# Performance work log

Measured on AMD Instinct MI355X. Metric: run time of the kernel, lower is better.

Reference implementation:

```python
import jax, jax.numpy as jnp
import numpy as np

D_MODEL = 384
HEADS = 8
DIM_HEAD = D_MODEL // HEADS
IH = IW = 32
N = IH * IW
D_FF = 1536
EPS = 1e-5


def _relative_index():
    # replicates torch buffer construction (meshgrid 'ij')
    gy, gx = np.meshgrid(np.arange(IH), np.arange(IW), indexing='ij')
    coords = np.stack([gy, gx]).reshape(2, -1)              # [2, N]
    rel = coords[:, :, None] - coords[:, None, :]           # [2, N, N]
    rel[0] += IH - 1
    rel[1] += IW - 1
    rel[0] *= 2 * IW - 1
    return (rel[0] + rel[1]).reshape(-1)                    # [N*N] int


def setup_inputs() -> dict:
    key = jax.random.key(0)
    ks = jax.random.split(key, 16)
    s = 0.02
    return {
        'src': jax.random.normal(ks[0], (8, N, D_MODEL), jnp.float32),
        'pos': jax.random.normal(ks[1], (8, N, D_MODEL), jnp.float32),
        'rel_bias_table': jax.random.normal(ks[2], ((2 * IH - 1) * (2 * IW - 1), HEADS), jnp.float32) * s,
        'Wq': jax.random.normal(ks[3], (D_MODEL, D_MODEL), jnp.float32) * s,
        'Wk': jax.random.normal(ks[4], (D_MODEL, D_MODEL), jnp.float32) * s,
        'Wv': jax.random.normal(ks[5], (D_MODEL, D_MODEL), jnp.float32) * s,
        'Wo': jax.random.normal(ks[6], (D_MODEL, D_MODEL), jnp.float32) * s,
        'bo': jnp.zeros((D_MODEL,), jnp.float32),
        'W1': jax.random.normal(ks[7], (D_MODEL, D_FF), jnp.float32) * s,
        'b1': jnp.zeros((D_FF,), jnp.float32),
        'W2': jax.random.normal(ks[8], (D_FF, D_MODEL), jnp.float32) * s,
        'b2': jnp.zeros((D_MODEL,), jnp.float32),
        'g1': jnp.ones((D_MODEL,), jnp.float32),
        'be1': jnp.zeros((D_MODEL,), jnp.float32),
        'g2': jnp.ones((D_MODEL,), jnp.float32),
        'be2': jnp.zeros((D_MODEL,), jnp.float32),
    }


def _layernorm(x, g, b):
    mu = jnp.mean(x, -1, keepdims=True)
    var = jnp.var(x, -1, keepdims=True)
    return (x - mu) * jax.lax.rsqrt(var + EPS) * g + b


def _heads(x):
    b, n, _ = x.shape
    return x.reshape(b, n, HEADS, DIM_HEAD).transpose(0, 2, 1, 3)  # [b,h,n,d]


def reference(src, pos, rel_bias_table, Wq, Wk, Wv, Wo, bo, W1, b1, W2, b2, g1, be1, g2, be2):
    rel_idx = _relative_index()
    qk_in = src + pos
    q = _heads(qk_in @ Wq)
    k = _heads(qk_in @ Wk)
    v = _heads(src @ Wv)
    # relative bias: [heads, n, n]
    bias = rel_bias_table[rel_idx].reshape(N, N, HEADS).transpose(2, 0, 1)
    # relative_bias_x = (x^T @ bias)^T  ==  sum_m bias[h,m,n] * x[b,h,m,d]
    q = q + jnp.einsum('hmn,bhmd->bhnd', bias, q)
    k = k + jnp.einsum('hmn,bhmd->bhnd', bias, k)
    v = v + jnp.einsum('hmn,bhmd->bhnd', bias, v)
    scale = DIM_HEAD ** -0.5
    dots = jnp.einsum('bhnd,bhmd->bhnm', q, k) * scale
    attn = jax.nn.softmax(dots, axis=-1)
    out = jnp.einsum('bhnm,bhmd->bhnd', attn, v)
    out = out.transpose(0, 2, 1, 3).reshape(src.shape[0], N, D_MODEL)
    out = out @ Wo + bo
    x = _layernorm(src + out, g1, be1)
    ff = jax.nn.gelu(x @ W1 + b1, approximate=False) @ W2 + b2
    return _layernorm(x + ff, g2, be2)
```

## Files before the change

kernel.cpp:

```cpp
#include <hip/hip_runtime.h>
#include <math.h>

#define D_MODEL 384
#define HEADS 8
#define DIM_HEAD 48
#define NTOK 1024
#define BATCH 8
#define D_FF 1536
#define LN_EPS 1e-5f

typedef unsigned short u16;
typedef unsigned int u32;
typedef unsigned long long u64;
typedef short short8 __attribute__((ext_vector_type(8)));
typedef float f32x4 __attribute__((ext_vector_type(4)));

union F8 { short8 v; u64 q[2]; u16 u[8]; uint4 u4; };

__device__ __forceinline__ u16 f2bf(float f) {
    union { float f; unsigned u; } c; c.f = f;
    unsigned r = c.u + 0x7FFFu + ((c.u >> 16) & 1u);
    return (u16)(r >> 16);
}
__device__ __forceinline__ float bf2f(u16 u) {
    union { unsigned u; float f; } c; c.u = ((unsigned)u) << 16; return c.f;
}

__global__ __launch_bounds__(256) void add_cast_kernel(
        const float4* __restrict__ a, const float4* __restrict__ b,
        ushort4* __restrict__ o1, ushort4* __restrict__ o2, int n4) {
    int i = blockIdx.x * blockDim.x + threadIdx.x;
    if (i >= n4) return;
    float4 x = a[i], y = b[i];
    ushort4 u1, u2;
    u1.x = f2bf(x.x + y.x); u1.y = f2bf(x.y + y.y); u1.z = f2bf(x.z + y.z); u1.w = f2bf(x.w + y.w);
    u2.x = f2bf(x.x); u2.y = f2bf(x.y); u2.z = f2bf(x.z); u2.w = f2bf(x.w);
    o1[i] = u1; o2[i] = u2;
}

__global__ __launch_bounds__(256) void castT4_kernel(
        const float* __restrict__ i0, const float* __restrict__ i1,
        const float* __restrict__ i2, const float* __restrict__ i3,
        u16* __restrict__ o0, u16* __restrict__ o1,
        u16* __restrict__ o2, u16* __restrict__ o3) {
    const float* in  = (blockIdx.z == 0) ? i0 : (blockIdx.z == 1) ? i1 : (blockIdx.z == 2) ? i2 : i3;
    u16*         out = (blockIdx.z == 0) ? o0 : (blockIdx.z == 1) ? o1 : (blockIdx.z == 2) ? o2 : o3;
    __shared__ float t[32][33];
    int c0 = blockIdx.x * 32, r0 = blockIdx.y * 32;
    int tx = threadIdx.x, ty = threadIdx.y;
    for (int i = ty; i < 32; i += 8)
        t[i][tx] = in[(long)(r0 + i) * 384 + c0 + tx];
    __syncthreads();
    for (int i = ty; i < 32; i += 8)
        out[(long)(c0 + i) * 384 + r0 + tx] = f2bf(t[tx][i]);
}

__global__ __launch_bounds__(256) void castT_kernel(
        const float* __restrict__ in, u16* __restrict__ out, int R, int C) {
    __shared__ float t[32][33];
    int c0 = blockIdx.x * 32, r0 = blockIdx.y * 32;
    int tx = threadIdx.x, ty = threadIdx.y;
    for (int i = ty; i < 32; i += 8)
        t[i][tx] = in[(long)(r0 + i) * C + c0 + tx];
    __syncthreads();
    for (int i = ty; i < 32; i += 8)
        out[(long)(c0 + i) * R + r0 + tx] = f2bf(t[tx][i]);
}

__global__ __launch_bounds__(256) void biasT_bf16_kernel(const float* __restrict__ table,
                                                         u16* __restrict__ BT) {
    long i = (long)blockIdx.x * blockDim.x + threadIdx.x;
    const long total = (long)HEADS * NTOK * NTOK;
    if (i >= total) return;
    int m = (int)(i & 1023);
    int n = (int)((i >> 10) & 1023);
    int h = (int)(i >> 20);
    int dy = (m >> 5) - (n >> 5) + 31;
    int dx = (m & 31) - (n & 31) + 31;
    BT[i] = f2bf(table[(dy * 63 + dx) * HEADS + h]);
}

template<int OUTMODE, bool HAS_BIAS, bool HAS_RES, bool GELU_>
__global__ __launch_bounds__(256) void mgemm_kernel(
        const u16* __restrict__ Ab, const u16* __restrict__ Btb,
        float* __restrict__ Cf, u16* __restrict__ Cb, u16* __restrict__ Ct,
        const float* __restrict__ bias, const float* __restrict__ Rb,
        int M, int Kd, int Nd, int lda, int ldbt, int ldc, int ldr) {
    const u16* A  = Ab;
    const u16* Bt = Btb;

    __shared__ u16 As[64][40];
    __shared__ u16 Bs[64][40];
    int tid = threadIdx.x;
    int wave = tid >> 6, lane = tid & 63, g = lane >> 4, l15 = lane & 15;
    int wm = wave >> 1, wn = wave & 1;
    int row0 = blockIdx.y * 64, col0 = blockIdx.x * 64;

    f32x4 acc[2][2] = {};

    int sr = tid >> 2, sch = tid & 3;
    const u16* aSrc = A + (long)(row0 + sr) * lda + sch * 8;
    const u16* bSrc = Bt + (long)(col0 + sr) * ldbt + sch * 8;

    for (int k0 = 0; k0 < Kd; k0 += 32) {
        {
            uint4 va = *(const uint4*)(aSrc + k0);
            uint4 vb = *(const uint4*)(bSrc + k0);
            *(u64*)&As[sr][sch * 8]     = ((const u64*)&va)[0];
            *(u64*)&As[sr][sch * 8 + 4] = ((const u64*)&va)[1];
            *(u64*)&Bs[sr][sch * 8]     = ((const u64*)&vb)[0];
            *(u64*)&Bs[sr][sch * 8 + 4] = ((const u64*)&vb)[1];
        }
        __syncthreads();
        F8 af[2], bfr[2];
#pragma unroll
        for (int fm = 0; fm < 2; ++fm) {
            int r = wm * 32 + fm * 16 + l15;
            af[fm].q[0] = *(const u64*)&As[r][g * 8];
            af[fm].q[1] = *(const u64*)&As[r][g * 8 + 4];
        }
#pragma unroll
        for (int fn = 0; fn < 2; ++fn) {
            int c = wn * 32 + fn * 16 + l15;
            bfr[fn].q[0] = *(const u64*)&Bs[c][g * 8];
            bfr[fn].q[1] = *(const u64*)&Bs[c][g * 8 + 4];
        }
#pragma unroll
        for (int fm = 0; fm < 2; ++fm)
#pragma unroll
            for (int fn = 0; fn < 2; ++fn)
                acc[fm][fn] = __builtin_amdgcn_mfma_f32_16x16x32_bf16(
                    af[fm].v, bfr[fn].v, acc[fm][fn], 0, 0, 0);
        __syncthreads();
    }

#pragma unroll
    for (int fm = 0; fm < 2; ++fm) {
        int rbase = row0 + wm * 32 + fm * 16 + g * 4;
#pragma unroll
        for (int fn = 0; fn < 2; ++fn) {
            int c = col0 + wn * 32 + fn * 16 + l15;
            if (c < Nd) {
                float bv = HAS_BIAS ? bias[c] : 0.f;
                float vs[4];
#pragma unroll
                for (int r = 0; r < 4; ++r) {
                    float v = acc[fm][fn][r] + bv;
                    if (HAS_RES) v += Rb[(long)(rbase + r) * ldr + c];
                    if (GELU_)   v = 0.5f * v * (1.f + erff(v * 0.70710678118654752f));
                    vs[r] = v;
                    if (OUTMODE & 1) Cf[(long)(rbase + r) * ldc + c] = v;
                    if (OUTMODE & 2) Cb[(long)(rbase + r) * ldc + c] = f2bf(v);
                }
                if (OUTMODE & 8) {
                    int hh2 = (c * 683) >> 15; int dd = c - hh2 * 48;
                    int bb2 = rbase >> 10;     int mm = rbase & 1023;
                    ushort4 o;
                    o.x = f2bf(vs[0]); o.y = f2bf(vs[1]); o.z = f2bf(vs[2]); o.w = f2bf(vs[3]);
                    *(ushort4*)&Ct[(long)hh2 * 393216 + (long)(bb2 * 48 + dd) * 1024 + mm] = o;
                }
            }
        }
    }
}

__global__ __launch_bounds__(256) void bias3_kernel(
        const u16* __restrict__ BT, const u16* __restrict__ QtH,
        const u16* __restrict__ KtH, const u16* __restrict__ VtH,
        u16* __restrict__ Q2H, u16* __restrict__ K2H, u16* __restrict__ V2T) {
    int bid = blockIdx.x;
    int widx = (bid & 7) * 96 + (bid >> 3);
    int h = widx / 96;
    int rem = widx - h * 96;
    int ry = rem / 6, cx = rem - ry * 6;
    const long hb = (long)h * 393216;
    const u16* A = BT + (long)h * 1048576;
    __shared__ u16 As[64][40];
    __shared__ u16 Bq[64][40], Bk[64][40], Bv[64][40];
    int tid = threadIdx.x, wave = tid >> 6, lane = tid & 63, g = lane >> 4, l15 = lane & 15;
    int wm = wave >> 1, wn = wave & 1;
    int row0 = ry * 64, col0 = cx * 64;
    f32x4 acc[3][2][2] = {};
    int sr = tid >> 2, sch = tid & 3;
    const u16* aSrc = A   + (long)(row0 + sr) * 1024 + sch * 8;
    const u16* qSrc = QtH + hb + (long)(col0 + sr) * 1024 + sch * 8;
    const u16* kSrc = KtH + hb + (long)(col0 + sr) * 1024 + sch * 8;
    const u16* vSrc = VtH + hb + (long)(col0 + sr) * 1024 + sch * 8;

    for (int k0 = 0; k0 < 1024; k0 += 32) {
        uint4 va = *(const uint4*)(aSrc + k0);
        uint4 vq = *(const uint4*)(qSrc + k0);
        uint4 vk = *(const uint4*)(kSrc + k0);
        uint4 vv = *(const uint4*)(vSrc + k0);
        *(u64*)&As[sr][sch * 8] = ((const u64*)&va)[0]; *(u64*)&As[sr][sch * 8 + 4] = ((const u64*)&va)[1];
        *(u64*)&Bq[sr][sch * 8] = ((const u64*)&vq)[0]; *(u64*)&Bq[sr][sch * 8 + 4] = ((const u64*)&vq)[1];
        *(u64*)&Bk[sr][sch * 8] = ((const u64*)&vk)[0]; *(u64*)&Bk[sr][sch * 8 + 4] = ((const u64*)&vk)[1];
        *(u64*)&Bv[sr][sch * 8] = ((const u64*)&vv)[0]; *(u64*)&Bv[sr][sch * 8 + 4] = ((const u64*)&vv)[1];
        __syncthreads();
        F8 af0, af1, b0, b1;
        af0.q[0] = *(const u64*)&As[wm * 32 + l15][g * 8];
        af0.q[1] = *(const u64*)&As[wm * 32 + l15][g * 8 + 4];
        af1.q[0] = *(const u64*)&As[wm * 32 + 16 + l15][g * 8];
        af1.q[1] = *(const u64*)&As[wm * 32 + 16 + l15][g * 8 + 4];
        b0.q[0] = *(const u64*)&Bq[wn * 32 + l15][g * 8];
        b0.q[1] = *(const u64*)&Bq[wn * 32 + l15][g * 8 + 4];
        b1.q[0] = *(const u64*)&Bq[wn * 32 + 16 + l15][g * 8];
        b1.q[1] = *(const u64*)&Bq[wn * 32 + 16 + l15][g * 8 + 4];
        acc[0][0][0] = __builtin_amdgcn_mfma_f32_16x16x32_bf16(af0.v, b0.v, acc[0][0][0], 0, 0, 0);
        acc[0][0][1] = __builtin_amdgcn_mfma_f32_16x16x32_bf16(af0.v, b1.v, acc[0][0][1], 0, 0, 0);
        acc[0][1][0] = __builtin_amdgcn_mfma_f32_16x16x32_bf16(af1.v, b0.v, acc[0][1][0], 0, 0, 0);
        acc[0][1][1] = __builtin_amdgcn_mfma_f32_16x16x32_bf16(af1.v, b1.v, acc[0][1][1], 0, 0, 0);
        b0.q[0] = *(const u64*)&Bk[wn * 32 + l15][g * 8];
        b0.q[1] = *(const u64*)&Bk[wn * 32 + l15][g * 8 + 4];
        b1.q[0] = *(const u64*)&Bk[wn * 32 + 16 + l15][g * 8];
        b1.q[1] = *(const u64*)&Bk[wn * 32 + 16 + l15][g * 8 + 4];
        acc[1][0][0] = __builtin_amdgcn_mfma_f32_16x16x32_bf16(af0.v, b0.v, acc[1][0][0], 0, 0, 0);
        acc[1][0][1] = __builtin_amdgcn_mfma_f32_16x16x32_bf16(af0.v, b1.v, acc[1][0][1], 0, 0, 0);
        acc[1][1][0] = __builtin_amdgcn_mfma_f32_16x16x32_bf16(af1.v, b0.v, acc[1][1][0], 0, 0, 0);
        acc[1][1][1] = __builtin_amdgcn_mfma_f32_16x16x32_bf16(af1.v, b1.v, acc[1][1][1], 0, 0, 0);
        b0.q[0] = *(const u64*)&Bv[wn * 32 + l15][g * 8];
        b0.q[1] = *(const u64*)&Bv[wn * 32 + l15][g * 8 + 4];
        b1.q[0] = *(const u64*)&Bv[wn * 32 + 16 + l15][g * 8];
        b1.q[1] = *(const u64*)&Bv[wn * 32 + 16 + l15][g * 8 + 4];
        acc[2][0][0] = __builtin_amdgcn_mfma_f32_16x16x32_bf16(af0.v, b0.v, acc[2][0][0], 0, 0, 0);
        acc[2][0][1] = __builtin_amdgcn_mfma_f32_16x16x32_bf16(af0.v, b1.v, acc[2][0][1], 0, 0, 0);
        acc[2][1][0] = __builtin_amdgcn_mfma_f32_16x16x32_bf16(af1.v, b0.v, acc[2][1][0], 0, 0, 0);
        acc[2][1][1] = __builtin_amdgcn_mfma_f32_16x16x32_bf16(af1.v, b1.v, acc[2][1][1], 0, 0, 0);
        __syncthreads();
    }

    const float qsc = 0.14433756729740643f * 1.4426950408889634f;
#pragma unroll
    for (int fm = 0; fm < 2; ++fm) {
        int rbase = row0 + wm * 32 + fm * 16 + g * 4;
#pragma unroll
        for (int fn = 0; fn < 2; ++fn) {
            int c = col0 + wn * 32 + fn * 16 + l15;
            int b2 = (c * 683) >> 15, d = c - b2 * 48;
            long bh = (long)h * 8 + b2;
            ushort4 rq = *(const ushort4*)&QtH[hb + (long)c * 1024 + rbase];
            ushort4 rk = *(const ushort4*)&KtH[hb + (long)c * 1024 + rbase];
            ushort4 rv = *(const ushort4*)&VtH[hb + (long)c * 1024 + rbase];
            const u16* rqa = (const u16*)&rq;
            const u16* rka = (const u16*)&rk;
            const u16* rva = (const u16*)&rv;
            int ks = d >> 5, g3 = (d >> 3) & 3, e = d & 7;
            long qbase = ((bh * 64 + (rbase >> 4)) * 8 + ks * 4 + g3) * 128
                       + (rbase & 15) * 8 + e;
            ushort4 vo;
            u16* voa = (u16*)&vo;
#pragma unroll
            for (int r = 0; r < 4; ++r) {
                float qv = acc[0][fm][fn][r] + bf2f(rqa[r]);
                Q2H[qbase + r * 8] = f2bf(qv * qsc);
                float kv = acc[1][fm][fn][r] + bf2f(rka[r]);
                K2H[qbase + r * 8] = f2bf(kv);
                voa[r] = f2bf(acc[2][fm][fn][r] + bf2f(rva[r]));
            }
            long vaddr = ((((bh * 16 + (rbase >> 6)) * 3 + (d >> 4)) * 2
                          + ((rbase >> 5) & 1)) * 4 + ((rbase >> 3) & 3)) * 128
                       + (d & 15) * 8 + (rbase & 7);
            *(ushort4*)&V2T[vaddr] = vo;
            if (d < 16) {
                long pbase = ((bh * 64 + (rbase >> 4)) * 8 + 4 + 2 + (d >> 3)) * 128
                           + (rbase & 15) * 8 + (d & 7);
#pragma unroll
                for (int r = 0; r < 4; ++r) {
                    Q2H[pbase + r * 8] = 0;
                    K2H[pbase + r * 8] = 0;
                }
            }
        }
    }
}

__global__ __launch_bounds__(256, 4) void attn_mfma_kernel(
        const u16* __restrict__ Q2H, const u16* __restrict__ K2H,
        const u16* __restrict__ V2T, u16* __restrict__ O) {
    int bid = blockIdx.x;
    int widx = (bid & 7) * 512 + (bid >> 3);
    int qb = widx & 63;
    int h  = (widx >> 6) & 7;
    int b  = widx >> 9;
    int tid = threadIdx.x, wave = tid >> 6, lane = tid & 63, g = lane >> 4, l15 = lane & 15;

    __shared__ char smem[13824];
    u16   (*Pl)[16][72]  = (u16(*)[16][72])smem;
    float (*Oc)[16][52]  = (float(*)[16][52])smem;
    float (*MLc)[16][2]  = (float(*)[16][2])(smem + 13312);
    const int sw = ((l15 >> 3) & 1) << 5;
    const int loff = (g * 16 + l15) * 8;

    const long bh = (long)(h * 8 + b);
    const u16* qtile = Q2H + (bh * 64 + qb) * 1024;
    F8 qf0, qf1;
    qf0.u4 = *(const uint4*)(qtile + loff);
    qf1.u4 = *(const uint4*)(qtile + 512 + loff);

    f32x4 oacc[3] = {};
    float runm = -1e30f, runl = 0.f;

#pragma unroll
    for (int it = 0; it < 4; ++it) {
        f32x4 s[4] = {};
#pragma unroll
        for (int mt = 0; mt < 4; ++mt) {
            const u16* ktile = K2H + (bh * 64 + wave * 16 + it * 4 + mt) * 1024;
            F8 kf0, kf1;
            kf0.u4 = *(const uint4*)(ktile + loff);
            kf1.u4 = *(const uint4*)(ktile + 512 + loff);
            s[mt] = __builtin_amdgcn_mfma_f32_16x16x32_bf16(kf0.v, qf0.v, s[mt], 0, 0, 0);
            s[mt] = __builtin_amdgcn_mfma_f32_16x16x32_bf16(kf1.v, qf1.v, s[mt], 0, 0, 0);
        }

        const u16* vtile = V2T + (bh * 16 + wave * 4 + it) * 3072;
        F8 vf[3][2];
#pragma unroll
        for (int dt = 0; dt < 3; ++dt)
#pragma unroll
            for (int ks = 0; ks < 2; ++ks)
                vf[dt][ks].u4 = *(const uint4*)(vtile + (dt * 2 + ks) * 512 + loff);

        float p[16];
#pragma unroll
        for (int i = 0; i < 16; ++i) p[i] = s[i >> 2][i & 3];
        float pm[8];
#pragma unroll
        for (int i = 0; i < 8; ++i) pm[i] = fmaxf(p[i], p[i + 8]);
#pragma unroll
        for (int st = 4; st > 0; st >>= 1)
#pragma unroll
            for (int i = 0; i < st; ++i) pm[i] = fmaxf(pm[i], pm[i + st]);
        float tmax = pm[0];
        tmax = fmaxf(tmax, __shfl_xor(tmax, 16));
        tmax = fmaxf(tmax, __shfl_xor(tmax, 32));
        if (!__all(tmax <= runm + 8.0f)) {
            float nm = fmaxf(runm, tmax);
            float corr = __builtin_amdgcn_exp2f(runm - nm);
            runm = nm; runl *= corr;
#pragma unroll
            for (int dt = 0; dt < 3; ++dt) {
                oacc[dt][0] *= corr; oacc[dt][1] *= corr;
                oacc[dt][2] *= corr; oacc[dt][3] *= corr;
            }
        }
        float ps = 0.f;
#pragma unroll
        for (int i = 0; i < 16; ++i) { p[i] = __builtin_amdgcn_exp2f(p[i] - runm); ps += p[i]; }
        ps += __shfl_xor(ps, 16);
        ps += __shfl_xor(ps, 32);
        runl += ps;

#pragma unroll
        for (int mt = 0; mt < 4; ++mt) {
            u32 wa, wb;
            asm("v_cvt_pk_bf16_f32 %0, %1, %2" : "=v"(wa) : "v"(p[mt * 4]), "v"(p[mt * 4 + 1]));
            asm("v_cvt_pk_bf16_f32 %0, %1, %2" : "=v"(wb) : "v"(p[mt * 4 + 2]), "v"(p[mt * 4 + 3]));
            *(u64*)&Pl[wave][l15][(mt * 16 + g * 4) ^ sw] = ((u64)wb << 32) | wa;
        }
        F8 pb[2];
#pragma unroll
        for (int ks = 0; ks < 2; ++ks) {
            pb[ks].q[0] = *(const u64*)&Pl[wave][l15][(ks * 32 + g * 8) ^ sw];
            pb[ks].q[1] = *(const u64*)&Pl[wave][l15][((ks * 32 + g * 8) + 4) ^ sw];
        }

#pragma unroll
        for (int dt = 0; dt < 3; ++dt) {
            oacc[dt] = __builtin_amdgcn_mfma_f32_16x16x32_bf16(vf[dt][0].v, pb[0].v, oacc[dt], 0, 0, 0);
            oacc[dt] = __builtin_amdgcn_mfma_f32_16x16x32_bf16(vf[dt][1].v, pb[1].v, oacc[dt], 0, 0, 0);
        }
    }

    __syncthreads();
#pragma unroll
    for (int dt = 0; dt < 3; ++dt)
#pragma unroll
        for (int r = 0; r < 4; ++r)
            Oc[wave][l15][dt * 16 + g * 4 + r] = oacc[dt][r];
    if (g == 0) { MLc[wave][l15][0] = runm; MLc[wave][l15][1] = runl; }
    __syncthreads();

    if (wave == 0) {
        float mm[4], cc[4];
#pragma unroll
        for (int w = 0; w < 4; ++w) mm[w] = MLc[w][l15][0];
        float M = fmaxf(fmaxf(mm[0], mm[1]), fmaxf(mm[2], mm[3]));
        float LL = 0.f;
#pragma unroll
        for (int w = 0; w < 4; ++w) {
            cc[w] = __builtin_amdgcn_exp2f(mm[w] - M);
            LL += cc[w] * MLc[w][l15][1];
        }
        float inv = 1.f / LL;
        u16* op = O + ((long)b * NTOK + qb * 16 + l15) * D_MODEL + h * DIM_HEAD;
#pragma unroll
        for (int dt = 0; dt < 3; ++dt) {
            ushort4 o;
#pragma unroll
            for (int r = 0; r < 4; ++r) {
                int d = dt * 16 + g * 4 + r;
                float v = cc[0] * Oc[0][l15][d] + cc[1] * Oc[1][l15][d]
                        + cc[2] * Oc[2][l15][d] + cc[3] * Oc[3][l15][d];
                ((u16*)&o)[r] = f2bf(v * inv);
            }
            *(ushort4*)(op + dt * 16 + g * 4) = o;
        }
    }
}

__global__ __launch_bounds__(128) void ln_kernel(
        const float* __restrict__ X, const float* __restrict__ Rb,
        const float* __restrict__ g, const float* __restrict__ be,
        float* __restrict__ O, u16* __restrict__ Obf, int hasRes) {
    int row = blockIdx.x;
    int tid = threadIdx.x;
    const float* x = X + (long)row * D_MODEL;
    float v[3];
#pragma unroll
    for (int l = 0; l < 3; ++l) {
        int c = tid + l * 128;
        v[l] = x[c];
        if (hasRes) v[l] += Rb[(long)row * D_MODEL + c];
    }
    __shared__ float red[128];
    float s = v[0] + v[1] + v[2];
    red[tid] = s; __syncthreads();
    for (int st = 64; st > 0; st >>= 1) {
        if (tid < st) red[tid] += red[tid + st];
        __syncthreads();
    }
    float mean = red[0] * (1.f / 384.f);
    __syncthreads();
    float sq = 0.f;
#pragma unroll
    for (int l = 0; l < 3; ++l) { float d = v[l] - mean; sq += d * d; }
    red[tid] = sq; __syncthreads();
    for (int st = 64; st > 0; st >>= 1) {
        if (tid < st) red[tid] += red[tid + st];
        __syncthreads();
    }
    float rstd = rsqrtf(red[0] * (1.f / 384.f) + LN_EPS);
#pragma unroll
    for (int l = 0; l < 3; ++l) {
        int c = tid + l * 128;
        float o = (v[l] - mean) * rstd * g[c] + be[c];
        O[(long)row * D_MODEL + c] = o;
        if (Obf) Obf[(long)row * D_MODEL + c] = f2bf(o);
    }
}

extern "C" void kernel_launch(void* const* d_in, const int* in_sizes, int n_in,
                              void* d_out, int out_size, void* d_ws, size_t ws_size,
                              hipStream_t stream) {
    const float* src   = (const float*)d_in[0];
    const float* pos   = (const float*)d_in[1];
    const float* table = (const float*)d_in[2];
    const float* Wq  = (const float*)d_in[3];
    const float* Wk  = (const float*)d_in[4];
    const float* Wv  = (const float*)d_in[5];
    const float* Wo  = (const float*)d_in[6];
    const float* bo  = (const float*)d_in[7];
    const float* W1  = (const float*)d_in[8];
    const float* b1  = (const float*)d_in[9];
    const float* W2  = (const float*)d_in[10];
    const float* b2  = (const float*)d_in[11];
    const float* g1  = (const float*)d_in[12];
    const float* be1 = (const float*)d_in[13];
    const float* g2  = (const float*)d_in[14];
    const float* be2 = (const float*)d_in[15];
    float* out = (float*)d_out;
    u16* ws = (u16*)d_ws;

    const long SZ = (long)BATCH * NTOK * D_MODEL;

    u16* WqT  = ws + 0;
    u16* WkT  = ws + 147456;
    u16* WvT  = ws + 294912;
    u16* WoT  = ws + 442368;
    u16* W1T  = ws + 589824;
    u16* W2T  = ws + 1179648;
    u16* QKin = ws + 1769472;
    u16* SRCB = ws + 4915200;
    u16* QtH  = ws + 8060928;
    u16* KtH  = ws + 11206656;
    u16* VtH  = ws + 14352384;
    u16* BT   = ws + 17498112;
    u16* ATT  = ws + 17498112;
    u16* Q2H  = ws + 25886720;
    u16* K2H  = ws + 30081024;
    u16* V2T  = ws + 34275328;
    float* Of  = (float*)(ws + 8060928);
    float* xf  = (float*)(ws + 14352384);
    u16*   xbf = QKin;
    u16*   hbf = Q2H;
    float* ff  = (float*)(ws + 8060928);

    add_cast_kernel<<<(int)(SZ / 4 + 255) / 256, 256, 0, stream>>>(
        (const float4*)src, (const float4*)pos, (ushort4*)QKin, (ushort4*)SRCB, (int)(SZ / 4));
    dim3 tb(32, 8);
    castT4_kernel<<<dim3(12, 12, 4), tb, 0, stream>>>(Wq, Wk, Wv, Wo, WqT, WkT, WvT, WoT);
    castT_kernel<<<dim3(48, 12), tb, 0, stream>>>(W1, W1T, 384, 1536);
    castT_kernel<<<dim3(12, 48), tb, 0, stream>>>(W2, W2T, 1536, 384);
    biasT_bf16_kernel<<<32768, 256, 0, stream>>>(table, BT);
    mgemm_kernel<8, false, false, false><<<dim3(12, 128, 1), 256, 0, stream>>>(
        QKin, WqT, nullptr, nullptr, QtH, nullptr, nullptr,
        8192, 384, 768, 384, 384, 0, 0);
    mgemm_kernel<8, false, false, false><<<dim3(6, 128, 1), 256, 0, stream>>>(
        SRCB, WvT, nullptr, nullptr, VtH, nullptr, nullptr,
        8192, 384, 384, 384, 384, 0, 0);
    bias3_kernel<<<768, 256, 0, stream>>>(BT, QtH, KtH, VtH, Q2H, K2H, V2T);
    attn_mfma_kernel<<<4096, 256, 0, stream>>>(Q2H, K2H, V2T, ATT);
    mgemm_kernel<1, true, true, false><<<dim3(6, 128, 1), 256, 0, stream>>>(
        ATT, WoT, Of, nullptr, nullptr, bo, src,
        8192, 384, 384, 384, 384, 384, 384);
    ln_kernel<<<8192, 128, 0, stream>>>(Of, nullptr, g1, be1, xf, xbf, 0);
    mgemm_kernel<2, true, false, true><<<dim3(24, 128, 1), 256, 0, stream>>>(
        xbf, W1T, nullptr, hbf, nullptr, b1, nullptr,
        8192, 384, 1536, 384, 384, 1536, 0);
    mgemm_kernel<1, true, true, false><<<dim3(6, 128, 1), 256, 0, stream>>>(
        hbf, W2T, ff, nullptr, nullptr, b2, xf,
        8192, 1536, 384, 1536, 1536, 384, 384);
    ln_kernel<<<8192, 128, 0, stream>>>(ff, nullptr, g2, be2, out, nullptr, 0);
}
```

Measured before the change: 232.1 us.

## Use 128x128 GEMM tiles with direct global-to-LDS loads

Replaces the 64x64 bf16 MFMA GEMM with a 128x128 tile version in which each wave computes a 4x4 grid of 16x16 fragments. Operand tiles are staged with global_load_lds, which writes straight into unpadded LDS instead of going through registers. The goal is more operand reuse per load and fewer instructions for staging. The cost is far fewer blocks (as few as 192 for the N=384 GEMMs on a 256-CU part), possible LDS bank conflicts from the unpadded layout, and the loss of the column bounds check. The attention kernel also gains an explicit lgkmcnt wait and a sched_barrier between writing P to LDS and reading it back.

```diff
diff --git a/kernel.cpp b/kernel.cpp
--- a/kernel.cpp
+++ b/kernel.cpp
@@ -24,6 +24,11 @@
 }
 __device__ __forceinline__ float bf2f(u16 u) {
     union { unsigned u; float f; } c; c.u = ((unsigned)u) << 16; return c.f;
+}
+__device__ __forceinline__ void gload_lds16(const u16* g, u16* l) {
+    __builtin_amdgcn_global_load_lds(
+        (const __attribute__((address_space(1))) void*)g,
+        (__attribute__((address_space(3))) void*)l, 16, 0, 0);
 }
 
 __global__ __launch_bounds__(256) void add_cast_kernel(
@@ -81,84 +86,75 @@
 }
 
 template<int OUTMODE, bool HAS_BIAS, bool HAS_RES, bool GELU_>
-__global__ __launch_bounds__(256) void mgemm_kernel(
+__global__ __launch_bounds__(256) void mgemm128_kernel(
         const u16* __restrict__ Ab, const u16* __restrict__ Btb,
         float* __restrict__ Cf, u16* __restrict__ Cb, u16* __restrict__ Ct,
         const float* __restrict__ bias, const float* __restrict__ Rb,
-        int M, int Kd, int Nd, int lda, int ldbt, int ldc, int ldr) {
-    const u16* A  = Ab;
-    const u16* Bt = Btb;
-
-    __shared__ u16 As[64][40];
-    __shared__ u16 Bs[64][40];
-    int tid = threadIdx.x;
-    int wave = tid >> 6, lane = tid & 63, g = lane >> 4, l15 = lane & 15;
+        int Kd, int lda, int ldbt, int ldc, int ldr) {
+    __shared__ u16 As[128 * 32];
+    __shared__ u16 Bs[128 * 32];
+    int tid = threadIdx.x, wave = tid >> 6, lane = tid & 63, g = lane >> 4, l15 = lane & 15;
     int wm = wave >> 1, wn = wave & 1;
-    int row0 = blockIdx.y * 64, col0 = blockIdx.x * 64;
-
-    f32x4 acc[2][2] = {};
-
-    int sr = tid >> 2, sch = tid & 3;
-    const u16* aSrc = A + (long)(row0 + sr) * lda + sch * 8;
-    const u16* bSrc = Bt + (long)(col0 + sr) * ldbt + sch * 8;
+    int row0 = blockIdx.y * 128, col0 = blockIdx.x * 128;
+
+    f32x4 acc[4][4] = {};
+
+    int sr = lane >> 2, sk = lane & 3;
+    const u16* aG0 = Ab  + (long)(row0 + wave * 16 + sr) * lda  + sk * 8;
+    const u16* aG1 = Ab  + (long)(row0 + (wave + 4) * 16 + sr) * lda  + sk * 8;
+    const u16* bG0 = Btb + (long)(col0 + wave * 16 + sr) * ldbt + sk * 8;
+    const u16* bG1 = Btb + (long)(col0 + (wave + 4) * 16 + sr) * ldbt + sk * 8;
+    u16* asW0 = As + (wave * 16) * 32;
+    u16* asW1 = As + ((wave + 4) * 16) * 32;
+    u16* bsW0 = Bs + (wave * 16) * 32;
+    u16* bsW1 = Bs + ((wave + 4) * 16) * 32;
 
     for (int k0 = 0; k0 < Kd; k0 += 32) {
-        {
-            uint4 va = *(const uint4*)(aSrc + k0);
-            uint4 vb = *(const uint4*)(bSrc + k0);
-            *(u64*)&As[sr][sch * 8]     = ((const u64*)&va)[0];
-            *(u64*)&As[sr][sch * 8 + 4] = ((const u64*)&va)[1];
-            *(u64*)&Bs[sr][sch * 8]     = ((const u64*)&vb)[0];
-            *(u64*)&Bs[sr][sch * 8 + 4] = ((const u64*)&vb)[1];
-        }
+        gload_lds16(aG0 + k0, asW0);
+        gload_lds16(aG1 + k0, asW1);
+        gload_lds16(bG0 + k0, bsW0);
+        gload_lds16(bG1 + k0, bsW1);
+        asm volatile("s_waitcnt vmcnt(0)" ::: "memory");
         __syncthreads();
-        F8 af[2], bfr[2];
-#pragma unroll
-        for (int fm = 0; fm < 2; ++fm) {
-            int r = wm * 32 + fm * 16 + l15;
-            af[fm].q[0] = *(const u64*)&As[r][g * 8];
-            af[fm].q[1] = *(const u64*)&As[r][g * 8 + 4];
-        }
-#pragma unroll
-        for (int fn = 0; fn < 2; ++fn) {
-            int c = wn * 32 + fn * 16 + l15;
-            bfr[fn].q[0] = *(const u64*)&Bs[c][g * 8];
-            bfr[fn].q[1] = *(const u64*)&Bs[c][g * 8 + 4];
-        }
-#pragma unroll
-        for (int fm = 0; fm < 2; ++fm)
-#pragma unroll
-            for (int fn = 0; fn < 2; ++fn)
+        F8 af[4], bfr[4];
+#pragma unroll
+        for (int fm = 0; fm < 4; ++fm)
+            af[fm].u4 = *(const uint4*)&As[(wm * 64 + fm * 16 + l15) * 32 + g * 8];
+#pragma unroll
+        for (int fn = 0; fn < 4; ++fn)
+            bfr[fn].u4 = *(const uint4*)&Bs[(wn * 64 + fn * 16 + l15) * 32 + g * 8];
+#pragma unroll
+        for (int fm = 0; fm < 4; ++fm)
+#pragma unroll
+            for (int fn = 0; fn < 4; ++fn)
                 acc[fm][fn] = __builtin_amdgcn_mfma_f32_16x16x32_bf16(
                     af[fm].v, bfr[fn].v, acc[fm][fn], 0, 0, 0);
         __syncthreads();
     }
 
 #pragma unroll
-    for (int fm = 0; fm < 2; ++fm) {
-        int rbase = row0 + wm * 32 + fm * 16 + g * 4;
-#pragma unroll
-        for (int fn = 0; fn < 2; ++fn) {
-            int c = col0 + wn * 32 + fn * 16 + l15;
-            if (c < Nd) {
-                float bv = HAS_BIAS ? bias[c] : 0.f;
-                float vs[4];
-#pragma unroll
-                for (int r = 0; r < 4; ++r) {
-                    float v = acc[fm][fn][r] + bv;
-                    if (HAS_RES) v += Rb[(long)(rbase + r) * ldr + c];
-                    if (GELU_)   v = 0.5f * v * (1.f + erff(v * 0.70710678118654752f));
-                    vs[r] = v;
-                    if (OUTMODE & 1) Cf[(long)(rbase + r) * ldc + c] = v;
-                    if (OUTMODE & 2) Cb[(long)(rbase + r) * ldc + c] = f2bf(v);
-                }
-                if (OUTMODE & 8) {
-                    int hh2 = (c * 683) >> 15; int dd = c - hh2 * 48;
-                    int bb2 = rbase >> 10;     int mm = rbase & 1023;
-                    ushort4 o;
-                    o.x = f2bf(vs[0]); o.y = f2bf(vs[1]); o.z = f2bf(vs[2]); o.w = f2bf(vs[3]);
-                    *(ushort4*)&Ct[(long)hh2 * 393216 + (long)(bb2 * 48 + dd) * 1024 + mm] = o;
-                }
+    for (int fm = 0; fm < 4; ++fm) {
+        int rbase = row0 + wm * 64 + fm * 16 + g * 4;
+#pragma unroll
+        for (int fn = 0; fn < 4; ++fn) {
+            int c = col0 + wn * 64 + fn * 16 + l15;
+            float bv = HAS_BIAS ? bias[c] : 0.f;
+            float vs[4];
+#pragma unroll
+            for (int r = 0; r < 4; ++r) {
+                float v = acc[fm][fn][r] + bv;
+                if (HAS_RES) v += Rb[(long)(rbase + r) * ldr + c];
+                if (GELU_)   v = 0.5f * v * (1.f + erff(v * 0.70710678118654752f));
+                vs[r] = v;
+                if (OUTMODE & 1) Cf[(long)(rbase + r) * ldc + c] = v;
+                if (OUTMODE & 2) Cb[(long)(rbase + r) * ldc + c] = f2bf(v);
+            }
+            if (OUTMODE & 8) {
+                int hh2 = (c * 683) >> 15; int dd = c - hh2 * 48;
+                int bb2 = rbase >> 10;     int mm = rbase & 1023;
+                ushort4 o;
+                o.x = f2bf(vs[0]); o.y = f2bf(vs[1]); o.z = f2bf(vs[2]); o.w = f2bf(vs[3]);
+                *(ushort4*)&Ct[(long)hh2 * 393216 + (long)(bb2 * 48 + dd) * 1024 + mm] = o;
             }
         }
     }
@@ -358,6 +354,8 @@
             asm("v_cvt_pk_bf16_f32 %0, %1, %2" : "=v"(wb) : "v"(p[mt * 4 + 2]), "v"(p[mt * 4 + 3]));
             *(u64*)&Pl[wave][l15][(mt * 16 + g * 4) ^ sw] = ((u64)wb << 32) | wa;
         }
+        asm volatile("s_waitcnt lgkmcnt(0)" ::: "memory");
+        __builtin_amdgcn_sched_barrier(0);
         F8 pb[2];
 #pragma unroll
         for (int ks = 0; ks < 2; ++ks) {
@@ -503,23 +501,23 @@
     castT_kernel<<<dim3(48, 12), tb, 0, stream>>>(W1, W1T, 384, 1536);
     castT_kernel<<<dim3(12, 48), tb, 0, stream>>>(W2, W2T, 1536, 384);
     biasT_bf16_kernel<<<32768, 256, 0, stream>>>(table, BT);
-    mgemm_kernel<8, false, false, false><<<dim3(12, 128, 1), 256, 0, stream>>>(
+    mgemm128_kernel<8, false, false, false><<<dim3(6, 64), 256, 0, stream>>>(
         QKin, WqT, nullptr, nullptr, QtH, nullptr, nullptr,
-        8192, 384, 768, 384, 384, 0, 0);
-    mgemm_kernel<8, false, false, false><<<dim3(6, 128, 1), 256, 0, stream>>>(
+        384, 384, 384, 0, 0);
+    mgemm128_kernel<8, false, false, false><<<dim3(3, 64), 256, 0, stream>>>(
         SRCB, WvT, nullptr, nullptr, VtH, nullptr, nullptr,
-        8192, 384, 384, 384, 384, 0, 0);
+        384, 384, 384, 0, 0);
     bias3_kernel<<<768, 256, 0, stream>>>(BT, QtH, KtH, VtH, Q2H, K2H, V2T);
     attn_mfma_kernel<<<4096, 256, 0, stream>>>(Q2H, K2H, V2T, ATT);
-    mgemm_kernel<1, true, true, false><<<dim3(6, 128, 1), 256, 0, stream>>>(
+    mgemm128_kernel<1, true, true, false><<<dim3(3, 64), 256, 0, stream>>>(
         ATT, WoT, Of, nullptr, nullptr, bo, src,
-        8192, 384, 384, 384, 384, 384, 384);
+        384, 384, 384, 384, 384);
     ln_kernel<<<8192, 128, 0, stream>>>(Of, nullptr, g1, be1, xf, xbf, 0);
-    mgemm_kernel<2, true, false, true><<<dim3(24, 128, 1), 256, 0, stream>>>(
+    mgemm128_kernel<2, true, false, true><<<dim3(12, 64), 256, 0, stream>>>(
         xbf, W1T, nullptr, hbf, nullptr, b1, nullptr,
-        8192, 384, 1536, 384, 384, 1536, 0);
-    mgemm_kernel<1, true, true, false><<<dim3(6, 128, 1), 256, 0, stream>>>(
+        384, 384, 384, 1536, 0);
+    mgemm128_kernel<1, true, true, false><<<dim3(3, 64), 256, 0, stream>>>(
         hbf, W2T, ff, nullptr, nullptr, b2, xf,
-        8192, 1536, 384, 1536, 1536, 384, 384);
+        1536, 1536, 1536, 384, 384);
     ln_kernel<<<8192, 128, 0, stream>>>(ff, nullptr, g2, be2, out, nullptr, 0);
 }
```

After: 239.7 us. +3.3%, slower.
